# Kernel tuning notes

Measured on AMD Instinct MI355X. Metric: run time of the kernel, lower is better.

Reference implementation:

```python
import jax, jax.numpy as jnp
import numpy as np

N_HEAD = 16
LN_EPS = 1e-5


def _layernorm(x, g, b):
    mu = jnp.mean(x, axis=-1, keepdims=True)
    var = jnp.mean(jnp.square(x - mu), axis=-1, keepdims=True)
    return (x - mu) * jax.lax.rsqrt(var + LN_EPS) * g + b


def setup_inputs() -> dict:
    key = jax.random.key(0)
    ks = jax.random.split(key, 8)
    B, T, C = 2, 2048, 1024
    Dff = 4 * C
    s = 0.02
    return {
        "x": jax.random.normal(ks[0], (B, T, C), jnp.float32),
        "wq": jax.random.normal(ks[1], (C, C), jnp.float32) * s,
        "wk": jax.random.normal(ks[2], (C, C), jnp.float32) * s,
        "wv": jax.random.normal(ks[3], (C, C), jnp.float32) * s,
        "w_proj": jax.random.normal(ks[4], (C, C), jnp.float32) * s,
        "b_proj": jnp.zeros((C,), jnp.float32),
        "w1": jax.random.normal(ks[5], (C, Dff), jnp.float32) * s,
        "b1": jnp.zeros((Dff,), jnp.float32),
        "w2": jax.random.normal(ks[6], (Dff, C), jnp.float32) * s,
        "b2": jnp.zeros((C,), jnp.float32),
        "g1": jnp.ones((C,), jnp.float32),
        "be1": jnp.zeros((C,), jnp.float32),
        "g2": jnp.ones((C,), jnp.float32),
        "be2": jnp.zeros((C,), jnp.float32),
    }


def reference(x, wq, wk, wv, w_proj, b_proj, w1, b1, w2, b2, g1, be1, g2, be2):
    B, T, C = x.shape
    H = N_HEAD
    hd = C // H
    # QKV projections (all heads folded into one matmul each), -> [B,H,T,hd]
    q = (x @ wq).reshape(B, T, H, hd).transpose(0, 2, 1, 3)
    k = (x @ wk).reshape(B, T, H, hd).transpose(0, 2, 1, 3)
    v = (x @ wv).reshape(B, T, H, hd).transpose(0, 2, 1, 3)
    # scaled causal attention; scale = head_size ** -0.5 as in torch source
    scores = jnp.einsum("bhqd,bhkd->bhqk", q, k) * (hd ** -0.5)
    causal = jnp.tril(jnp.ones((T, T), bool))
    scores = jnp.where(causal, scores, jnp.finfo(scores.dtype).min)
    wei = jax.nn.softmax(scores, axis=-1)
    attn = jnp.einsum("bhqk,bhkd->bhqd", wei, v)  # [B,H,T,hd]
    attn = attn.transpose(0, 2, 1, 3).reshape(B, T, C)
    y = attn @ w_proj + b_proj
    # post-LN residuals as in Block.forward
    x = _layernorm(x + y, g1, be1)
    y = jnp.maximum(x @ w1 + b1, 0.0) @ w2 + b2
    x = _layernorm(x + y, g2, be2)
    return x
```

## Files before the change

### kernel.cpp

```cpp
#include <hip/hip_runtime.h>
#include <hip/hip_bf16.h>


typedef __attribute__((ext_vector_type(8))) short bf16x8;
typedef __attribute__((ext_vector_type(4))) float f32x4;
typedef __attribute__((ext_vector_type(4))) short short4v;

__device__ inline short f2bf(float f) {
    __hip_bfloat16 h = __float2bfloat16(f);
    return *reinterpret_cast<short*>(&h);
}
__device__ inline float bf2f(short s) {
    union { unsigned u; float f; } c;
    c.u = ((unsigned)(unsigned short)s) << 16;
    return c.f;
}

__global__ __launch_bounds__(256) void mega_prep(const float* __restrict__ x,
                                                 short* __restrict__ x_bf,
                                                 const float* __restrict__ wq,
                                                 const float* __restrict__ wk,
                                                 const float* __restrict__ wv,
                                                 const float* __restrict__ wp,
                                                 short* __restrict__ wqT,
                                                 short* __restrict__ wkT,
                                                 short* __restrict__ wvT,
                                                 short* __restrict__ wpT,
                                                 const float* __restrict__ w1,
                                                 short* __restrict__ w1T,
                                                 const float* __restrict__ w2,
                                                 short* __restrict__ w2T,
                                                 float scaleq) {
    const int blk = blockIdx.x;
    const int tid = threadIdx.x;
    if (blk < 4096) {
        const int i = blk * 256 + tid;
        float4 v = *(const float4*)(x + (size_t)i * 4);
        short4v o = { f2bf(v.x), f2bf(v.y), f2bf(v.z), f2bf(v.w) };
        *(short4v*)(x_bf + (size_t)i * 4) = o;
        return;
    }
    __shared__ short tile[32][33];
    const int tx = tid & 31, ty = tid >> 5;
    const float* in;
    short* out;
    int R, C, bx, by;
    float scale = 1.0f;
    if (blk < 8192) {
        const int b2 = blk - 4096;
        const int z = b2 >> 10;
        const int rem = b2 & 1023;
        bx = rem & 31; by = rem >> 5;
        R = 1024; C = 1024;
        in = z == 0 ? wq : z == 1 ? wk : z == 2 ? wv : wp;
        out = z == 0 ? wqT : z == 1 ? wkT : z == 2 ? wvT : wpT;
        if (z == 0) scale = scaleq;
    } else if (blk < 12288) {
        const int rem = blk - 8192;
        bx = rem & 127; by = rem >> 7;
        R = 1024; C = 4096;
        in = w1; out = w1T;
    } else {
        const int rem = blk - 12288;
        bx = rem & 31; by = rem >> 5;
        R = 4096; C = 1024;
        in = w2; out = w2T;
    }
    const int c0 = bx * 32, r0 = by * 32;
    for (int i = ty; i < 32; i += 8)
        tile[i][tx] = f2bf(in[(size_t)(r0 + i) * C + c0 + tx] * scale);
    __syncthreads();
    for (int i = ty; i < 32; i += 8)
        out[(size_t)(c0 + i) * R + r0 + tx] = tile[tx][i];
}

template <int BN, int BIAS, int RELU, int OUTBF>
__device__ __forceinline__ void gemm_core(const short* __restrict__ A,
                                          const short* __restrict__ BT,
                                          const float* __restrict__ bias,
                                          void* __restrict__ Cout,
                                          int N, int K, int lda, int ldb,
                                          int gx, int w,
                                          short* As, short* Bs, bool addbias) {
    constexpr int NI = BN / 32;
    const int tid = threadIdx.x;
    const int wid = tid >> 6;
    const int lane = tid & 63;
    const int wr = wid >> 1, wc = wid & 1;
    const int row0 = (w % gx) * 128;
    const int col0 = (w / gx) * BN;
    const int lr = lane & 15;
    const int lk = (lane >> 4) * 8;
    const int sr = lane >> 3;
    const int scs = ((lane & 7) * 8) ^ (sr * 8);
    const int rsw = (lr & 7) * 8;

    f32x4 acc[4][NI] = {};
    for (int k = 0; k < K; k += 64) {
#pragma unroll
        for (int c = 0; c < 4; ++c) {
            const int ch = wid + c * 4;
            const short* ga = A + (size_t)(row0 + ch * 8 + sr) * lda + k + scs;
            __builtin_amdgcn_global_load_lds(
                (const __attribute__((address_space(1))) unsigned int*)ga,
                (__attribute__((address_space(3))) unsigned int*)(As + ch * 512), 16, 0, 0);
        }
#pragma unroll
        for (int c = 0; c < BN / 32; ++c) {
            const int ch = wid + c * 4;
            const short* gb = BT + (size_t)(col0 + ch * 8 + sr) * ldb + k + scs;
            __builtin_amdgcn_global_load_lds(
                (const __attribute__((address_space(1))) unsigned int*)gb,
                (__attribute__((address_space(3))) unsigned int*)(Bs + ch * 512), 16, 0, 0);
        }
        __syncthreads();
#pragma unroll
        for (int kk = 0; kk < 64; kk += 32) {
            const int cof = (kk + lk) ^ rsw;
            bf16x8 a[4], b[NI];
#pragma unroll
            for (int m = 0; m < 4; ++m)
                a[m] = *(const bf16x8*)(As + (wr * 64 + m * 16 + lr) * 64 + cof);
#pragma unroll
            for (int n = 0; n < NI; ++n)
                b[n] = *(const bf16x8*)(Bs + (wc * (BN / 2) + n * 16 + lr) * 64 + cof);
#pragma unroll
            for (int m = 0; m < 4; ++m)
#pragma unroll
                for (int n = 0; n < NI; ++n)
                    acc[m][n] = __builtin_amdgcn_mfma_f32_16x16x32_bf16(a[m], b[n], acc[m][n], 0, 0, 0);
        }
        __syncthreads();
    }
#pragma unroll
    for (int m = 0; m < 4; ++m) {
        int row = row0 + wr * 64 + m * 16 + (lane >> 4) * 4;
#pragma unroll
        for (int n = 0; n < NI; ++n) {
            int col = col0 + wc * (BN / 2) + n * 16 + lr;
            float bv = (BIAS && addbias) ? bias[col] : 0.0f;
#pragma unroll
            for (int r = 0; r < 4; ++r) {
                float v = acc[m][n][r] + bv;
                if (RELU) v = fmaxf(v, 0.0f);
                if (OUTBF)
                    ((short*)Cout)[(size_t)(row + r) * N + col] = f2bf(v);
                else
                    ((float*)Cout)[(size_t)(row + r) * N + col] = v;
            }
        }
    }
}

template <int BN, int BIAS, int RELU, int OUTBF>
__global__ __launch_bounds__(256) void gemm_bt(const short* __restrict__ A,
                                               const short* __restrict__ BT,
                                               const float* __restrict__ bias,
                                               void* __restrict__ Cout,
                                               int N, int K, int lda, int ldb,
                                               void* __restrict__ Cout2) {
    __shared__ short As[128 * 64];
    __shared__ short Bs[BN * 64];
    const int kz = blockIdx.z;
    if (kz) { A += K; BT += K; Cout = Cout2; }
    const int gx = gridDim.x;
    int flat = blockIdx.x + gx * blockIdx.y;
    const int nwg = gx * gridDim.y;
    int w = flat;
    if ((nwg & 7) == 0) {
        const int q = nwg >> 3;
        w = (flat & 7) * q + (flat >> 3);
    }
    gemm_core<BN, BIAS, RELU, OUTBF>(A, BT, bias, Cout, N, K, lda, ldb, gx, w, As, Bs, kz == 0);
}

__global__ __launch_bounds__(256) void gemm_qkv_vt(const short* __restrict__ x_bf,
                                                   const short* __restrict__ wqkT,
                                                   const short* __restrict__ wvT,
                                                   short* __restrict__ qk,
                                                   short* __restrict__ Vt) {
    __shared__ short As[128 * 64];
    __shared__ short Bs[128 * 64];
    int flat = blockIdx.x;
    if (flat < 512) {
        const int w = (flat & 7) * 64 + (flat >> 3);
        gemm_core<128, 0, 0, 1>(x_bf, wqkT, nullptr, qk, 2048, 1024, 1024, 1024, 32, w, As, Bs, false);
    } else {
        flat -= 512;
        const int w = (flat & 7) * 32 + (flat >> 3);
        gemm_core<128, 0, 0, 1>(wvT, x_bf, nullptr, Vt, 4096, 1024, 1024, 1024, 8, w, As, Bs, false);
    }
}

#define STAGE_MLP1(KT, BF)                                                                  \
    do {                                                                                    \
        const int kof_ = (KT) * 64;                                                         \
        _Pragma("unroll") for (int l = 0; l < 4; ++l) {                                     \
            const int ch = wid * 4 + l;                                                     \
            const short* ga = A + (size_t)(row0 + ch * 8 + sr) * 1024 + kof_ + scs;         \
            __builtin_amdgcn_global_load_lds(                                               \
                (const __attribute__((address_space(1))) unsigned int*)ga,                  \
                (__attribute__((address_space(3))) unsigned int*)(&As[BF][ch * 512]), 16, 0, 0); \
            const short* gb = BT + (size_t)(col0 + ch * 8 + sr) * 1024 + kof_ + scs;        \
            __builtin_amdgcn_global_load_lds(                                               \
                (const __attribute__((address_space(1))) unsigned int*)gb,                  \
                (__attribute__((address_space(3))) unsigned int*)(&Bs[BF][ch * 512]), 16, 0, 0); \
        }                                                                                   \
    } while (0)

__global__ __launch_bounds__(512, 2) void gemm_mlp1(const short* __restrict__ A,
                                                    const short* __restrict__ BT,
                                                    const float* __restrict__ bias,
                                                    short* __restrict__ C) {
    __shared__ short As[2][256 * 64];
    __shared__ short Bs[2][256 * 64];
    const int tid = threadIdx.x;
    const int wid = tid >> 6;
    const int lane = tid & 63;
    const int wm = wid >> 2;
    const int wn = wid & 3;
    const int flat = blockIdx.x;
    const int w = (flat & 7) * 32 + (flat >> 3);
    const int row0 = (w & 15) * 256;
    const int col0 = (w >> 4) * 256;
    const int lr = lane & 15;
    const int lk = (lane >> 4) * 8;
    const int sr = lane >> 3;
    const int scs = ((lane & 7) * 8) ^ (sr * 8);
    const int rsw = (lr & 7) * 8;

    f32x4 acc[8][4] = {};

    STAGE_MLP1(0, 0);
    STAGE_MLP1(1, 1);

    const int NK = 16;
#pragma unroll 1
    for (int t = 0; t < NK; ++t) {
        const int c = t & 1;
        if (t == NK - 1)
            asm volatile("s_waitcnt vmcnt(0)" ::: "memory");
        else
            asm volatile("s_waitcnt vmcnt(8)" ::: "memory");
        __builtin_amdgcn_s_barrier();
        bf16x8 bfr[4][2];
#pragma unroll
        for (int fj = 0; fj < 4; ++fj)
#pragma unroll
            for (int ks = 0; ks < 2; ++ks)
                bfr[fj][ks] = *(const bf16x8*)(&Bs[c][(wn * 64 + fj * 16 + lr) * 64 +
                                                      ((ks * 32 + lk) ^ rsw)]);
#pragma unroll
        for (int p = 0; p < 4; ++p) {
            bf16x8 afr[2][2];
#pragma unroll
            for (int f = 0; f < 2; ++f)
#pragma unroll
                for (int ks = 0; ks < 2; ++ks)
                    afr[f][ks] = *(const bf16x8*)(&As[c][(wm * 128 + (p * 2 + f) * 16 + lr) * 64 +
                                                         ((ks * 32 + lk) ^ rsw)]);
            asm volatile("s_waitcnt lgkmcnt(0)" ::: "memory");
            __builtin_amdgcn_sched_barrier(0);
            if (p == 3) {
                __builtin_amdgcn_s_barrier();
                if (t + 2 < NK) STAGE_MLP1(t + 2, c);
            }
            __builtin_amdgcn_s_setprio(1);
#pragma unroll
            for (int f = 0; f < 2; ++f)
#pragma unroll
                for (int fj = 0; fj < 4; ++fj)
#pragma unroll
                    for (int ks = 0; ks < 2; ++ks)
                        acc[p * 2 + f][fj] = __builtin_amdgcn_mfma_f32_16x16x32_bf16(
                            afr[f][ks], bfr[fj][ks], acc[p * 2 + f][fj], 0, 0, 0);
            __builtin_amdgcn_s_setprio(0);
            __builtin_amdgcn_s_barrier();
        }
    }
#pragma unroll
    for (int fi = 0; fi < 8; ++fi) {
        const int row = row0 + wm * 128 + fi * 16 + (lane >> 4) * 4;
#pragma unroll
        for (int fj = 0; fj < 4; ++fj) {
            const int col = col0 + wn * 64 + fj * 16 + lr;
            const float bv = bias[col];
#pragma unroll
            for (int r = 0; r < 4; ++r) {
                float v = fmaxf(acc[fi][fj][r] + bv, 0.0f);
                C[(size_t)(row + r) * 4096 + col] = f2bf(v);
            }
        }
    }
}

#define ATT_T 2048
#define ATT_QKS 2048
#define ATT_BT 4096

#define LOADK(KF, KB)                                                                     \
    do {                                                                                  \
        const int k0_ = (KB) * 64;                                                        \
        _Pragma("unroll") for (int t = 0; t < 4; ++t) {                                   \
            const size_t krow_ = (size_t)(b * ATT_T + k0_ + 16 * t + lr) * ATT_QKS + h * 64; \
            KF[t][0] = *(const bf16x8*)(Km + krow_ + g * 8);                              \
            KF[t][1] = *(const bf16x8*)(Km + krow_ + 32 + g * 8);                         \
        }                                                                                 \
    } while (0)

#define LOADV(VF, KB)                                                                     \
    do {                                                                                  \
        const int k0_ = (KB) * 64;                                                        \
        _Pragma("unroll") for (int n = 0; n < 4; ++n)                                     \
            _Pragma("unroll") for (int ks = 0; ks < 2; ++ks)                              \
                VF[n][ks] = *(const bf16x8*)(Vt + (size_t)(h * 64 + n * 16 + lr) * ATT_BT + \
                                             b * ATT_T + k0_ + ks * 32 + g * 8);          \
    } while (0)

#define COMPUTE(KF, VF, KB)                                                               \
    do {                                                                                  \
        const int k0_ = (KB) * 64;                                                        \
        const bool edge_ = (KB) == nfull;                                                 \
        _Pragma("unroll") for (int qs = 0; qs < 2; ++qs) {                                \
            f32x4 st[4];                                                                  \
            __builtin_amdgcn_s_setprio(1);                                                \
            _Pragma("unroll") for (int t = 0; t < 4; ++t) {                               \
                f32x4 s = {};                                                             \
                s = __builtin_amdgcn_mfma_f32_16x16x32_bf16(KF[t][0], aq[qs][0], s, 0, 0, 0); \
                s = __builtin_amdgcn_mfma_f32_16x16x32_bf16(KF[t][1], aq[qs][1], s, 0, 0, 0); \
                st[t] = s;                                                                \
            }                                                                             \
            __builtin_amdgcn_s_setprio(0);                                                \
            float rst[4];                                                                 \
            _Pragma("unroll") for (int t = 0; t < 4; ++t) {                               \
                short4v pw;                                                               \
                float pr[4];                                                              \
                _Pragma("unroll") for (int r = 0; r < 4; ++r) {                           \
                    float val = st[t][r];                                                 \
                    if (edge_ && (k0_ + 16 * t + g * 4 + r > qrow[qs])) val = -3e38f;     \
                    float p = exp2f(val);                                                 \
                    pr[r] = p;                                                            \
                    pw[r] = f2bf(p);                                                      \
                }                                                                         \
                rst[t] = (pr[0] + pr[1]) + (pr[2] + pr[3]);                               \
                *(short4v*)(&Plds[wid][qs][lr][16 * t + g * 4]) = pw;                     \
            }                                                                             \
            float rs = (rst[0] + rst[1]) + (rst[2] + rst[3]);                             \
            rs += __shfl_xor(rs, 16);                                                     \
            rs += __shfl_xor(rs, 32);                                                     \
            lrun[qs] += rs;                                                               \
        }                                                                                 \
        asm volatile("s_waitcnt lgkmcnt(0)" ::: "memory");                                \
        __builtin_amdgcn_sched_barrier(0);                                                \
        __builtin_amdgcn_s_setprio(1);                                                    \
        _Pragma("unroll") for (int qs = 0; qs < 2; ++qs)                                  \
            _Pragma("unroll") for (int ks = 0; ks < 2; ++ks) {                            \
                bf16x8 pf = *(const bf16x8*)(&Plds[wid][qs][lr][ks * 32 + g * 8]);        \
                _Pragma("unroll") for (int n = 0; n < 4; ++n)                             \
                    O[qs][n] = __builtin_amdgcn_mfma_f32_16x16x32_bf16(VF[n][ks], pf, O[qs][n], 0, 0, 0); \
            }                                                                             \
        __builtin_amdgcn_s_setprio(0);                                                    \
    } while (0)

__global__ __launch_bounds__(128) void flash_attn(const short* __restrict__ Q,
                                                  const short* __restrict__ Km,
                                                  const short* __restrict__ Vt,
                                                  short* __restrict__ Oout) {
    const int f = blockIdx.x;
    const int wid = threadIdx.x >> 6;
    const int lane = threadIdx.x & 63;
    const int lr = lane & 15;
    const int g = lane >> 4;
    const int xcd = f & 7;
    const int k = f >> 3;
    const int bh = xcd * 4 + (k & 3);
    const int b = bh >> 4;
    const int h = bh & 15;
    const int pair = (k >> 2) * 2 + wid;

    __shared__ __align__(16) short Plds[2][2][16][72];

#pragma unroll 1
    for (int job = 0; job < 2; ++job) {
        const int s = job ? (63 - pair) : pair;
        const int q0 = s << 5;
        const int qrow[2] = { q0 + lr, q0 + 16 + lr };
        const int nfull = s >> 1;

        bf16x8 aq[2][2];
#pragma unroll
        for (int qs = 0; qs < 2; ++qs)
#pragma unroll
            for (int ds = 0; ds < 2; ++ds)
                aq[qs][ds] = *(const bf16x8*)(Q + (size_t)(b * ATT_T + q0 + qs * 16 + lr) * ATT_QKS +
                                              h * 64 + ds * 32 + g * 8);

        f32x4 O[2][4] = {};
        float lrun[2] = { 0.0f, 0.0f };

        bf16x8 kfA[4][2], kfB[4][2], vf[4][2];
        LOADK(kfA, 0);
        int kb = 0;
        while (true) {
            LOADV(vf, kb);
            if (kb < nfull) LOADK(kfB, kb + 1);
            COMPUTE(kfA, vf, kb);
            ++kb;
            if (kb > nfull) break;
            LOADV(vf, kb);
            if (kb < nfull) LOADK(kfA, kb + 1);
            COMPUTE(kfB, vf, kb);
            ++kb;
            if (kb > nfull) break;
        }

#pragma unroll
        for (int qs = 0; qs < 2; ++qs) {
            const float inv = 1.0f / lrun[qs];
#pragma unroll
            for (int n = 0; n < 4; ++n) {
                short4v ov;
#pragma unroll
                for (int r = 0; r < 4; ++r) ov[r] = f2bf(O[qs][n][r] * inv);
                *(short4v*)(Oout + (size_t)(b * ATT_T + q0 + qs * 16 + lr) * 1024 +
                            h * 64 + n * 16 + g * 4) = ov;
            }
        }
    }
}

template <int XB>
__global__ __launch_bounds__(256) void resid_ln(const float* __restrict__ xf,
                                                const short* __restrict__ xb,
                                                const short* __restrict__ y,
                                                const short* __restrict__ yb,
                                                const float* __restrict__ g,
                                                const float* __restrict__ be,
                                                float* __restrict__ of,
                                                short* __restrict__ ob) {
    const int row = blockIdx.x;
    const int tid = threadIdx.x;
    const size_t base = (size_t)row * 1024 + tid * 4;
    float x0, x1, x2, x3;
    if (XB) {
        short4v xv = *(const short4v*)(xb + base);
        x0 = bf2f(xv[0]); x1 = bf2f(xv[1]); x2 = bf2f(xv[2]); x3 = bf2f(xv[3]);
    } else {
        float4 xv = *(const float4*)(xf + base);
        x0 = xv.x; x1 = xv.y; x2 = xv.z; x3 = xv.w;
    }
    short4v yv = *(const short4v*)(y + base);
    float h0 = x0 + bf2f(yv[0]), h1 = x1 + bf2f(yv[1]);
    float h2 = x2 + bf2f(yv[2]), h3 = x3 + bf2f(yv[3]);
    if (yb) {
        short4v bv2 = *(const short4v*)(yb + base);
        h0 += bf2f(bv2[0]); h1 += bf2f(bv2[1]); h2 += bf2f(bv2[2]); h3 += bf2f(bv2[3]);
    }
    float s = h0 + h1 + h2 + h3;
    float ss = h0 * h0 + h1 * h1 + h2 * h2 + h3 * h3;
#pragma unroll
    for (int d = 1; d < 64; d <<= 1) {
        s += __shfl_xor(s, d);
        ss += __shfl_xor(ss, d);
    }
    __shared__ float as_[4], ass_[4];
    if ((tid & 63) == 0) { as_[tid >> 6] = s; ass_[tid >> 6] = ss; }
    __syncthreads();
    s = as_[0] + as_[1] + as_[2] + as_[3];
    ss = ass_[0] + ass_[1] + ass_[2] + ass_[3];
    const float mu = s * (1.0f / 1024.0f);
    const float var = ss * (1.0f / 1024.0f) - mu * mu;
    const float rstd = rsqrtf(var + 1e-5f);
    float4 gv = *(const float4*)(g + tid * 4);
    float4 bv = *(const float4*)(be + tid * 4);
    float o0 = (h0 - mu) * rstd * gv.x + bv.x;
    float o1 = (h1 - mu) * rstd * gv.y + bv.y;
    float o2 = (h2 - mu) * rstd * gv.z + bv.z;
    float o3 = (h3 - mu) * rstd * gv.w + bv.w;
    if (of) {
        float4 ov = { o0, o1, o2, o3 };
        *(float4*)(of + base) = ov;
    }
    if (ob) {
        short4v obv = { f2bf(o0), f2bf(o1), f2bf(o2), f2bf(o3) };
        *(short4v*)(ob + base) = obv;
    }
}


extern "C" void kernel_launch(void* const* d_in, const int* in_sizes, int n_in,
                              void* d_out, int out_size, void* d_ws, size_t ws_size,
                              hipStream_t stream) {
    const float* x = (const float*)d_in[0];
    const float* wq = (const float*)d_in[1];
    const float* wk = (const float*)d_in[2];
    const float* wv = (const float*)d_in[3];
    const float* wp = (const float*)d_in[4];
    const float* bproj = (const float*)d_in[5];
    const float* w1 = (const float*)d_in[6];
    const float* b1 = (const float*)d_in[7];
    const float* w2 = (const float*)d_in[8];
    const float* b2 = (const float*)d_in[9];
    const float* g1 = (const float*)d_in[10];
    const float* be1 = (const float*)d_in[11];
    const float* g2 = (const float*)d_in[12];
    const float* be2 = (const float*)d_in[13];

    char* ws = (char*)d_ws;
    const size_t MB = 1024 * 1024;
    short* x_bf = (short*)(ws + 0);
    short* wqkT = (short*)(ws + 8 * MB);
    short* wqT = wqkT;
    short* wkT = (short*)(ws + 10 * MB);
    short* wvT = (short*)(ws + 12 * MB);
    short* w1T = (short*)(ws + 16 * MB);
    short* w2T = (short*)(ws + 24 * MB);
    short* qk  = (short*)(ws + 32 * MB);
    short* wpT = (short*)(ws + 48 * MB);
    short* Vt  = (short*)(ws + 56 * MB);
    short* hbf = (short*)(ws + 32 * MB);
    short* attn = (short*)(ws + 64 * MB);
    short* x1bf = (short*)(ws + 64 * MB);
    short* y1a = (short*)(ws + 72 * MB);
    short* y1b = (short*)(ws + 0);
    short* y2a = (short*)(ws + 72 * MB);
    short* y2b = (short*)(ws + 0);

    dim3 blk(256);
    const float SC = 0.125f * 1.44269504089f;

    mega_prep<<<dim3(16384), blk, 0, stream>>>(x, x_bf, wq, wk, wv, wp,
                                               wqT, wkT, wvT, wpT,
                                               w1, w1T, w2, w2T, SC);
    gemm_qkv_vt<<<dim3(768), blk, 0, stream>>>(x_bf, wqkT, wvT, qk, Vt);
    flash_attn<<<dim3(512), dim3(128), 0, stream>>>(qk, qk + 1024, Vt, attn);
    gemm_bt<64, 1, 0, 1><<<dim3(32, 16, 2), blk, 0, stream>>>(attn, wpT, bproj, y1a,
                                                              1024, 512, 1024, 1024, y1b);
    resid_ln<0><<<dim3(4096), blk, 0, stream>>>(x, nullptr, y1a, y1b, g1, be1,
                                                nullptr, x1bf);
    gemm_mlp1<<<dim3(256), dim3(512), 0, stream>>>(x1bf, w1T, b1, hbf);
    gemm_bt<64, 1, 0, 1><<<dim3(32, 16, 2), blk, 0, stream>>>(hbf, w2T, b2, y2a,
                                                              1024, 2048, 4096, 4096, y2b);
    resid_ln<1><<<dim3(4096), blk, 0, stream>>>(nullptr, x1bf, y2a, y2b, g2, be2,
                                                (float*)d_out, nullptr);
}
```

Before: 266.4 us.

## Reuse 256x256 MFMA GEMM core for QKV and split-K MLP2 GEMMs

Pulls the 256x256, 512-thread double-buffered GEMM body out of gemm_mlp1 into a templated core. The QKV/V-transpose projection now uses 192 large-tile blocks instead of 768 128x128 blocks. The second MLP GEMM uses the same core with a 4-way K split, and the final residual LayerNorm sums four bf16 partials instead of two. The aim is higher data reuse per block and the faster pipelined core, at the cost of fewer blocks than CUs for the QKV GEMM and extra partial-sum traffic for MLP2.

```diff
diff --git a/kernel.cpp b/kernel.cpp
--- a/kernel.cpp
+++ b/kernel.cpp
@@ -174,39 +174,107 @@
     gemm_core<BN, BIAS, RELU, OUTBF>(A, BT, bias, Cout, N, K, lda, ldb, gx, w, As, Bs, kz == 0);
 }
 
-__global__ __launch_bounds__(256) void gemm_qkv_vt(const short* __restrict__ x_bf,
-                                                   const short* __restrict__ wqkT,
-                                                   const short* __restrict__ wvT,
-                                                   short* __restrict__ qk,
-                                                   short* __restrict__ Vt) {
-    __shared__ short As[128 * 64];
-    __shared__ short Bs[128 * 64];
-    int flat = blockIdx.x;
-    if (flat < 512) {
-        const int w = (flat & 7) * 64 + (flat >> 3);
-        gemm_core<128, 0, 0, 1>(x_bf, wqkT, nullptr, qk, 2048, 1024, 1024, 1024, 32, w, As, Bs, false);
-    } else {
-        flat -= 512;
-        const int w = (flat & 7) * 32 + (flat >> 3);
-        gemm_core<128, 0, 0, 1>(wvT, x_bf, nullptr, Vt, 4096, 1024, 1024, 1024, 8, w, As, Bs, false);
-    }
-}
-
-#define STAGE_MLP1(KT, BF)                                                                  \
+#define STAGE256(KT, ASB, BSB)                                                              \
     do {                                                                                    \
         const int kof_ = (KT) * 64;                                                         \
         _Pragma("unroll") for (int l = 0; l < 4; ++l) {                                     \
             const int ch = wid * 4 + l;                                                     \
-            const short* ga = A + (size_t)(row0 + ch * 8 + sr) * 1024 + kof_ + scs;         \
+            const short* ga = A + (size_t)(row0 + ch * 8 + sr) * lda + kof_ + scs;          \
             __builtin_amdgcn_global_load_lds(                                               \
                 (const __attribute__((address_space(1))) unsigned int*)ga,                  \
-                (__attribute__((address_space(3))) unsigned int*)(&As[BF][ch * 512]), 16, 0, 0); \
-            const short* gb = BT + (size_t)(col0 + ch * 8 + sr) * 1024 + kof_ + scs;        \
+                (__attribute__((address_space(3))) unsigned int*)((ASB) + ch * 512), 16, 0, 0); \
+            const short* gb = BT + (size_t)(col0 + ch * 8 + sr) * ldb + kof_ + scs;         \
             __builtin_amdgcn_global_load_lds(                                               \
                 (const __attribute__((address_space(1))) unsigned int*)gb,                  \
-                (__attribute__((address_space(3))) unsigned int*)(&Bs[BF][ch * 512]), 16, 0, 0); \
+                (__attribute__((address_space(3))) unsigned int*)((BSB) + ch * 512), 16, 0, 0); \
         }                                                                                   \
     } while (0)
+
+template <int BIAS, int RELU>
+__device__ __forceinline__ void gemm256_core(const short* __restrict__ A,
+                                             const short* __restrict__ BT,
+                                             const float* __restrict__ bias,
+                                             short* __restrict__ C,
+                                             int N, int K, int lda, int ldb,
+                                             int row0, int col0, bool addbias,
+                                             short* As0, short* As1,
+                                             short* Bs0, short* Bs1) {
+    const int tid = threadIdx.x;
+    const int wid = tid >> 6;
+    const int lane = tid & 63;
+    const int wm = wid >> 2;
+    const int wn = wid & 3;
+    const int lr = lane & 15;
+    const int lk = (lane >> 4) * 8;
+    const int sr = lane >> 3;
+    const int scs = ((lane & 7) * 8) ^ (sr * 8);
+    const int rsw = (lr & 7) * 8;
+
+    f32x4 acc[8][4] = {};
+    STAGE256(0, As0, Bs0);
+    STAGE256(1, As1, Bs1);
+
+    const int NK = K >> 6;
+#pragma unroll 1
+    for (int t = 0; t < NK; ++t) {
+        short* Asc = (t & 1) ? As1 : As0;
+        short* Bsc = (t & 1) ? Bs1 : Bs0;
+        if (t == NK - 1)
+            asm volatile("s_waitcnt vmcnt(0)" ::: "memory");
+        else
+            asm volatile("s_waitcnt vmcnt(8)" ::: "memory");
+        __builtin_amdgcn_s_barrier();
+        bf16x8 bfr[4][2];
+#pragma unroll
+        for (int fj = 0; fj < 4; ++fj)
+#pragma unroll
+            for (int ks = 0; ks < 2; ++ks)
+                bfr[fj][ks] = *(const bf16x8*)(&Bsc[(wn * 64 + fj * 16 + lr) * 64 +
+                                                    ((ks * 32 + lk) ^ rsw)]);
+#pragma unroll
+        for (int p = 0; p < 4; ++p) {
+            bf16x8 afr[2][2];
+#pragma unroll
+            for (int f = 0; f < 2; ++f)
+#pragma unroll
+                for (int ks = 0; ks < 2; ++ks)
+                    afr[f][ks] = *(const bf16x8*)(&Asc[(wm * 128 + (p * 2 + f) * 16 + lr) * 64 +
+                                                       ((ks * 32 + lk) ^ rsw)]);
+            asm volatile("s_waitcnt lgkmcnt(0)" ::: "memory");
+            __builtin_amdgcn_sched_barrier(0);
+            if (p == 3) {
+                __builtin_amdgcn_s_barrier();
+                if (t + 2 < NK) STAGE256(t + 2, Asc, Bsc);
+            }
+            __builtin_amdgcn_s_setprio(1);
+#pragma unroll
+            for (int f = 0; f < 2; ++f)
+#pragma unroll
+                for (int fj = 0; fj < 4; ++fj)
+#pragma unroll
+                    for (int ks = 0; ks < 2; ++ks)
+                        acc[p * 2 + f][fj] = __builtin_amdgcn_mfma_f32_16x16x32_bf16(
+                            afr[f][ks], bfr[fj][ks], acc[p * 2 + f][fj], 0, 0, 0);
+            __builtin_amdgcn_s_setprio(0);
+            __builtin_amdgcn_s_barrier();
+        }
+    }
+#pragma unroll
+    for (int fi = 0; fi < 8; ++fi) {
+        const int row = row0 + wm * 128 + fi * 16 + (lane >> 4) * 4;
+#pragma unroll
+        for (int fj = 0; fj < 4; ++fj) {
+            const int col = col0 + wn * 64 + fj * 16 + lr;
+            const float bv = (BIAS && addbias) ? bias[col] : 0.0f;
+#pragma unroll
+            for (int r = 0; r < 4; ++r) {
+                float v = acc[fi][fj][r] + bv;
+                if (RELU) v = fmaxf(v, 0.0f);
+                C[(size_t)(row + r) * N + col] = f2bf(v);
+            }
+        }
+    }
+}
 
 __global__ __launch_bounds__(512, 2) void gemm_mlp1(const short* __restrict__ A,
                                                     const short* __restrict__ BT,
@@ -214,84 +282,55 @@
                                                     short* __restrict__ C) {
     __shared__ short As[2][256 * 64];
     __shared__ short Bs[2][256 * 64];
-    const int tid = threadIdx.x;
-    const int wid = tid >> 6;
-    const int lane = tid & 63;
-    const int wm = wid >> 2;
-    const int wn = wid & 3;
     const int flat = blockIdx.x;
     const int w = (flat & 7) * 32 + (flat >> 3);
     const int row0 = (w & 15) * 256;
     const int col0 = (w >> 4) * 256;
-    const int lr = lane & 15;
-    const int lk = (lane >> 4) * 8;
-    const int sr = lane >> 3;
-    const int scs = ((lane & 7) * 8) ^ (sr * 8);
-    const int rsw = (lr & 7) * 8;
-
-    f32x4 acc[8][4] = {};
-
-    STAGE_MLP1(0, 0);
-    STAGE_MLP1(1, 1);
-
-    const int NK = 16;
-#pragma unroll 1
-    for (int t = 0; t < NK; ++t) {
-        const int c = t & 1;
-        if (t == NK - 1)
-            asm volatile("s_waitcnt vmcnt(0)" ::: "memory");
-        else
-            asm volatile("s_waitcnt vmcnt(8)" ::: "memory");
-        __builtin_amdgcn_s_barrier();
-        bf16x8 bfr[4][2];
-#pragma unroll
-        for (int fj = 0; fj < 4; ++fj)
-#pragma unroll
-            for (int ks = 0; ks < 2; ++ks)
-                bfr[fj][ks] = *(const bf16x8*)(&Bs[c][(wn * 64 + fj * 16 + lr) * 64 +
-                                                      ((ks * 32 + lk) ^ rsw)]);
-#pragma unroll
-        for (int p = 0; p < 4; ++p) {
-            bf16x8 afr[2][2];
-#pragma unroll
-            for (int f = 0; f < 2; ++f)
-#pragma unroll
-                for (int ks = 0; ks < 2; ++ks)
-                    afr[f][ks] = *(const bf16x8*)(&As[c][(wm * 128 + (p * 2 + f) * 16 + lr) * 64 +
-                                                         ((ks * 32 + lk) ^ rsw)]);
-            asm volatile("s_waitcnt lgkmcnt(0)" ::: "memory");
-            __builtin_amdgcn_sched_barrier(0);
-            if (p == 3) {
-                __builtin_amdgcn_s_barrier();
-                if (t + 2 < NK) STAGE_MLP1(t + 2, c);
-            }
-            __builtin_amdgcn_s_setprio(1);
-#pragma unroll
-            for (int f = 0; f < 2; ++f)
-#pragma unroll
-                for (int fj = 0; fj < 4; ++fj)
-#pragma unroll
-                    for (int ks = 0; ks < 2; ++ks)
-                        acc[p * 2 + f][fj] = __builtin_amdgcn_mfma_f32_16x16x32_bf16(
-                            afr[f][ks], bfr[fj][ks], acc[p * 2 + f][fj], 0, 0, 0);
-            __builtin_amdgcn_s_setprio(0);
-            __builtin_amdgcn_s_barrier();
-        }
-    }
-#pragma unroll
-    for (int fi = 0; fi < 8; ++fi) {
-        const int row = row0 + wm * 128 + fi * 16 + (lane >> 4) * 4;
-#pragma unroll
-        for (int fj = 0; fj < 4; ++fj) {
-            const int col = col0 + wn * 64 + fj * 16 + lr;
-            const float bv = bias[col];
-#pragma unroll
-            for (int r = 0; r < 4; ++r) {
-                float v = fmaxf(acc[fi][fj][r] + bv, 0.0f);
-                C[(size_t)(row + r) * 4096 + col] = f2bf(v);
-            }
-        }
-    }
+    gemm256_core<1, 1>(A, BT, bias, C, 4096, 1024, 1024, 1024, row0, col0, true,
+                       As[0], As[1], Bs[0], Bs[1]);
+}
+
+__global__ __launch_bounds__(512, 2) void gemm_qkvvt(const short* __restrict__ x_bf,
+                                                     const short* __restrict__ wqkT,
+                                                     const short* __restrict__ wvT,
+                                                     short* __restrict__ qk,
+                                                     short* __restrict__ Vt) {
+    __shared__ short As[2][256 * 64];
+    __shared__ short Bs[2][256 * 64];
+    int flat = blockIdx.x;
+    if (flat < 128) {
+        const int w = (flat & 7) * 16 + (flat >> 3);
+        const int row0 = (w & 15) * 256;
+        const int col0 = (w >> 4) * 256;
+        gemm256_core<0, 0>(x_bf, wqkT, nullptr, qk, 2048, 1024, 1024, 1024,
+                           row0, col0, false, As[0], As[1], Bs[0], Bs[1]);
+    } else {
+        flat -= 128;
+        const int w = (flat & 7) * 8 + (flat >> 3);
+        const int row0 = (w & 3) * 256;
+        const int col0 = (w >> 2) * 256;
+        gemm256_core<0, 0>(wvT, x_bf, nullptr, Vt, 4096, 1024, 1024, 1024,
+                           row0, col0, false, As[0], As[1], Bs[0], Bs[1]);
+    }
+}
+
+__global__ __launch_bounds__(512, 2) void gemm_mlp2(const short* __restrict__ A,
+                                                    const short* __restrict__ BT,
+                                                    const float* __restrict__ bias,
+                                                    short* __restrict__ C0,
+                                                    short* __restrict__ C1,
+                                                    short* __restrict__ C2,
+                                                    short* __restrict__ C3) {
+    __shared__ short As[2][256 * 64];
+    __shared__ short Bs[2][256 * 64];
+    const int kz = blockIdx.z;
+    short* C = kz == 0 ? C0 : kz == 1 ? C1 : kz == 2 ? C2 : C3;
+    const int flat = blockIdx.x;
+    const int w = (flat & 7) * 8 + (flat >> 3);
+    const int row0 = (w & 15) * 256;
+    const int col0 = (w >> 4) * 256;
+    gemm256_core<1, 0>(A + kz * 1024, BT + kz * 1024, bias, C, 1024, 1024,
+                       4096, 4096, row0, col0, kz == 0, As[0], As[1], Bs[0], Bs[1]);
 }
 
 #define ATT_T 2048
@@ -434,6 +473,8 @@
                                                 const short* __restrict__ xb,
                                                 const short* __restrict__ y,
                                                 const short* __restrict__ yb,
+                                                const short* __restrict__ yc,
+                                                const short* __restrict__ yd,
                                                 const float* __restrict__ g,
                                                 const float* __restrict__ be,
                                                 float* __restrict__ of,
@@ -453,8 +494,16 @@
     float h0 = x0 + bf2f(yv[0]), h1 = x1 + bf2f(yv[1]);
     float h2 = x2 + bf2f(yv[2]), h3 = x3 + bf2f(yv[3]);
     if (yb) {
-        short4v bv2 = *(const short4v*)(yb + base);
-        h0 += bf2f(bv2[0]); h1 += bf2f(bv2[1]); h2 += bf2f(bv2[2]); h3 += bf2f(bv2[3]);
+        short4v v2 = *(const short4v*)(yb + base);
+        h0 += bf2f(v2[0]); h1 += bf2f(v2[1]); h2 += bf2f(v2[2]); h3 += bf2f(v2[3]);
+    }
+    if (yc) {
+        short4v v3 = *(const short4v*)(yc + base);
+        h0 += bf2f(v3[0]); h1 += bf2f(v3[1]); h2 += bf2f(v3[2]); h3 += bf2f(v3[3]);
+    }
+    if (yd) {
+        short4v v4 = *(const short4v*)(yd + base);
+        h0 += bf2f(v4[0]); h1 += bf2f(v4[1]); h2 += bf2f(v4[2]); h3 += bf2f(v4[3]);
     }
     float s = h0 + h1 + h2 + h3;
     float ss = h0 * h0 + h1 * h1 + h2 * h2 + h3 * h3;
@@ -525,6 +574,8 @@
     short* y1b = (short*)(ws + 0);
     short* y2a = (short*)(ws + 72 * MB);
     short* y2b = (short*)(ws + 0);
+    short* y2c = (short*)(ws + 8 * MB);
+    short* y2d = (short*)(ws + 16 * MB);
 
     dim3 blk(256);
     const float SC = 0.125f * 1.44269504089f;
@@ -532,15 +583,14 @@
     mega_prep<<<dim3(16384), blk, 0, stream>>>(x, x_bf, wq, wk, wv, wp,
                                                wqT, wkT, wvT, wpT,
                                                w1, w1T, w2, w2T, SC);
-    gemm_qkv_vt<<<dim3(768), blk, 0, stream>>>(x_bf, wqkT, wvT, qk, Vt);
+    gemm_qkvvt<<<dim3(192), dim3(512), 0, stream>>>(x_bf, wqkT, wvT, qk, Vt);
     flash_attn<<<dim3(512), dim3(128), 0, stream>>>(qk, qk + 1024, Vt, attn);
     gemm_bt<64, 1, 0, 1><<<dim3(32, 16, 2), blk, 0, stream>>>(attn, wpT, bproj, y1a,
                                                               1024, 512, 1024, 1024, y1b);
-    resid_ln<0><<<dim3(4096), blk, 0, stream>>>(x, nullptr, y1a, y1b, g1, be1,
-                                                nullptr, x1bf);
+    resid_ln<0><<<dim3(4096), blk, 0, stream>>>(x, nullptr, y1a, y1b, nullptr, nullptr,
+                                                g1, be1, nullptr, x1bf);
     gemm_mlp1<<<dim3(256), dim3(512), 0, stream>>>(x1bf, w1T, b1, hbf);
-    gemm_bt<64, 1, 0, 1><<<dim3(32, 16, 2), blk, 0, stream>>>(hbf, w2T, b2, y2a,
-                                                              1024, 2048, 4096, 4096, y2b);
-    resid_ln<1><<<dim3(4096), blk, 0, stream>>>(nullptr, x1bf, y2a, y2b, g2, be2,
-                                                (float*)d_out, nullptr);
-}
+    gemm_mlp2<<<dim3(64, 1, 4), dim3(512), 0, stream>>>(hbf, w2T, b2, y2a, y2b, y2c, y2d);
+    resid_ln<1><<<dim3(4096), blk, 0, stream>>>(nullptr, x1bf, y2a, y2b, y2c, y2d,
+                                                g2, be2, (float*)d_out, nullptr);
+}
```

New measurement: 253.4 us. -4.9%, faster.
